# Kernel optimization log

Hardware: AMD Instinct MI355X
Metric: run time of the kernel (lower is better)

Reference implementation:

```python
import jax, jax.numpy as jnp
import numpy as np

T = 3          # num_node_type
B = 8          # batch
N = 512        # max_doc_len
F_IN = 256     # in_features
F_OUT = 128    # out_features
NE = 10        # num_edge_type (embedding has NE+1 rows, row 0 = padding)
ALPHA = 0.2    # leaky relu slope
NEG = -9e15    # masked-score fill, same constant as torch source


def setup_inputs() -> dict:
    key = jax.random.key(0)
    ks = jax.random.split(key, 7)
    node_rep = jax.random.normal(ks[0], (B, N, F_IN), jnp.float32)
    node_type_mask_rep = jax.random.uniform(ks[1], (T, B, N, 1), jnp.float32)
    adj = jax.random.randint(ks[2], (B, N, N), 0, NE + 1, jnp.int32)
    W = jax.random.normal(ks[3], (T, F_IN, F_OUT), jnp.float32) * 0.05
    b = jnp.zeros((T, F_OUT), jnp.float32)
    # attention vector a in R^{2F} split into halves (GAT trick): a([h_i, x2_ij]) = h_i.a1 + x2_ij.a2 + a_b
    a1 = jax.random.normal(ks[4], (F_OUT,), jnp.float32) * 0.05
    a2 = jax.random.normal(ks[5], (F_OUT,), jnp.float32) * 0.05
    a_b = jnp.zeros((), jnp.float32)
    emb = jax.random.normal(ks[6], (NE + 1, F_OUT), jnp.float32) * 0.05
    emb = emb.at[0].set(0.0)  # padding_idx=0
    return {"node_rep": node_rep, "node_type_mask_rep": node_type_mask_rep,
            "adj": adj, "W": W, "b": b, "a1": a1, "a2": a2, "a_b": a_b, "emb": emb}


def reference(node_rep, node_type_mask_rep, adj, W, b, a1, a2, a_b, emb):
    # typed projection: h = sum_t (node_rep @ W_t + b_t) * mask_t   -> (B, N, F_OUT)
    h = jnp.sum((jnp.einsum('bni,tio->tbno', node_rep, W) + b[:, None, None, :])
                * node_type_mask_rep, axis=0)
    # edge-type embeddings: (B, N, N, F_OUT)
    E = emb[adj]
    # x_2[b,i,j] = h[b,j] + E[b,i,j]
    x2 = h[:, None, :, :] + E
    # score[b,i,j] = leakyrelu(a1.h_i + a2.x2_ij + a_b)  (decomposed concat-linear)
    s = (jnp.einsum('bif,f->bi', h, a1)[:, :, None]
         + jnp.einsum('bijf,f->bij', x2, a2) + a_b)
    s = jnp.where(s > 0, s, ALPHA * s)
    s = jnp.where(adj > 0, s, jnp.float32(NEG))
    attn = jax.nn.softmax(s, axis=2)
    # weighted sum over neighbors of x_2 (NOT h), then ELU
    out = jnp.einsum('bij,bijf->bif', attn, x2)
    return jax.nn.elu(out)
```

## Files before the change

### kernel.cpp

```cpp
#include <hip/hip_runtime.h>

constexpr int kB    = 8;
constexpr int kN    = 512;
constexpr int kFIN  = 256;
constexpr int kFOUT = 128;
constexpr int kNE   = 10;
constexpr int kBN   = kB * kN;
constexpr float kALPHA = 0.2f;
constexpr float kNEG   = -9e15f;

__global__ __launch_bounds__(512) void proj_kernel(
    const float* __restrict__ node_rep,
    const float* __restrict__ mask,
    const float* __restrict__ W,
    const float* __restrict__ bias,
    const float* __restrict__ a1,
    const float* __restrict__ a2,
    const float* __restrict__ a_b,
    const float* __restrict__ emb,
    float* __restrict__ h,
    float* __restrict__ s1,
    float* __restrict__ s2,
    float* __restrict__ emb_a2)
{
    __shared__ float xs[8][kFIN];
    __shared__ float parts[9][8][kFOUT];

    const int tid  = threadIdx.x;
    const int row0 = blockIdx.x * 8;
    const int o    = tid & 127;
    const int kq   = tid >> 7;

    {
        const int r = tid >> 6, q = tid & 63;
        *(float4*)&xs[r][q * 4] =
            *(const float4*)&node_rep[(size_t)(row0 + r) * kFIN + q * 4];
    }
    __syncthreads();

    float acc[3][8];
    #pragma unroll
    for (int t = 0; t < 3; ++t)
        #pragma unroll
        for (int r = 0; r < 8; ++r) acc[t][r] = 0.f;

    const float* Wo = W + o;
    #pragma unroll 2
    for (int i4 = 0; i4 < 16; ++i4) {
        const int kb = kq * 64 + i4 * 4;
        float4 xv[8];
        #pragma unroll
        for (int r = 0; r < 8; ++r)
            xv[r] = *(const float4*)&xs[r][kb];
        #pragma unroll
        for (int c = 0; c < 4; ++c) {
            const int k = kb + c;
            const float w0 = Wo[(0 * kFIN + k) * kFOUT];
            const float w1 = Wo[(1 * kFIN + k) * kFOUT];
            const float w2 = Wo[(2 * kFIN + k) * kFOUT];
            #pragma unroll
            for (int r = 0; r < 8; ++r) {
                const float x = ((const float*)&xv[r])[c];
                acc[0][r] = fmaf(w0, x, acc[0][r]);
                acc[1][r] = fmaf(w1, x, acc[1][r]);
                acc[2][r] = fmaf(w2, x, acc[2][r]);
            }
        }
    }

    if (kq > 0) {
        #pragma unroll
        for (int t = 0; t < 3; ++t)
            #pragma unroll
            for (int r = 0; r < 8; ++r)
                parts[(kq - 1) * 3 + t][r][o] = acc[t][r];
    }
    __syncthreads();

    if (kq == 0) {
        #pragma unroll
        for (int r = 0; r < 8; ++r) {
            const int row = row0 + r;
            float hv = 0.f;
            #pragma unroll
            for (int t = 0; t < 3; ++t) {
                const float s = acc[t][r] + parts[t][r][o] + parts[3 + t][r][o]
                              + parts[6 + t][r][o] + bias[t * kFOUT + o];
                hv = fmaf(mask[t * kBN + row], s, hv);
            }
            h[(size_t)row * kFOUT + o] = hv;
            parts[0][r][o] = hv;
        }
    }
    __syncthreads();

    {
        const int r = tid >> 6, lane = tid & 63;
        const float v0 = parts[0][r][lane];
        const float v1 = parts[0][r][64 + lane];
        float p1 = v0 * a1[lane] + v1 * a1[64 + lane];
        float p2 = v0 * a2[lane] + v1 * a2[64 + lane];
        #pragma unroll
        for (int off = 32; off; off >>= 1) {
            p1 += __shfl_down(p1, off);
            p2 += __shfl_down(p2, off);
        }
        if (lane == 0) {
            s1[row0 + r] = p1 + a_b[0];
            s2[row0 + r] = p2;
        }
    }

    if (blockIdx.x == 0 && tid < 176) {
        const int e = tid >> 4, l = tid & 15;
        float p = 0.f;
        #pragma unroll
        for (int k8 = 0; k8 < 8; ++k8)
            p += emb[e * kFOUT + l + k8 * 16] * a2[l + k8 * 16];
        #pragma unroll
        for (int off = 8; off; off >>= 1) p += __shfl_xor(p, off);
        if (l == 0) emb_a2[e] = p;
    }
}

__global__ __launch_bounds__(512) void attn_kernel(
    const int*   __restrict__ adj,
    const float* __restrict__ emb,
    const float* __restrict__ h,
    const float* __restrict__ s1,
    const float* __restrict__ s2,
    const float* __restrict__ emb_a2g,
    float* __restrict__ out)
{
    __shared__ float sc[8][kN + 4];
    __shared__ int   adjs[8][kN];
    __shared__ float s2s[kN];
    __shared__ float s1s[8];
    __shared__ float wsum[8][16];
    __shared__ float ea2[16];

    const int tid = threadIdx.x;
    const int b   = blockIdx.x >> 6;
    const int i0  = (blockIdx.x & 63) * 8;

    if (tid < 16) ea2[tid] = emb_a2g[tid];
    if (tid < 8)  s1s[tid] = s1[b * kN + i0 + tid];
    s2s[tid] = s2[b * kN + tid];
    __syncthreads();

    const int* adjb = adj + ((size_t)(b * kN + i0)) * kN;
    #pragma unroll
    for (int it = 0; it < 2; ++it) {
        const int idx = tid + it * 512;
        const int r = idx >> 7, jq = idx & 127;
        const int4   av  = *(const int4*)&adjb[(size_t)r * kN + jq * 4];
        const float4 s2v = *(const float4*)&s2s[jq * 4];
        const float  sr  = s1s[r];
        float4 sv;
        float s;
        s = sr + s2v.x + ea2[av.x]; s = s > 0.f ? s : kALPHA * s; sv.x = av.x > 0 ? s : kNEG;
        s = sr + s2v.y + ea2[av.y]; s = s > 0.f ? s : kALPHA * s; sv.y = av.y > 0 ? s : kNEG;
        s = sr + s2v.z + ea2[av.z]; s = s > 0.f ? s : kALPHA * s; sv.z = av.z > 0 ? s : kNEG;
        s = sr + s2v.w + ea2[av.w]; s = s > 0.f ? s : kALPHA * s; sv.w = av.w > 0 ? s : kNEG;
        *(float4*)&sc[r][jq * 4]  = sv;
        *(int4*)&adjs[r][jq * 4]  = av;
    }
    __syncthreads();

    {
        const int r = tid >> 6, lane = tid & 63;
        float v[8]; int av[8];
        #pragma unroll
        for (int k = 0; k < 8; ++k) {
            v[k]  = sc[r][lane + k * 64];
            av[k] = adjs[r][lane + k * 64];
        }
        float m = v[0];
        #pragma unroll
        for (int k = 1; k < 8; ++k) m = fmaxf(m, v[k]);
        #pragma unroll
        for (int off = 32; off; off >>= 1) m = fmaxf(m, __shfl_xor(m, off));
        float sum = 0.f;
        #pragma unroll
        for (int k = 0; k < 8; ++k) { v[k] = __expf(v[k] - m); sum += v[k]; }
        #pragma unroll
        for (int off = 32; off; off >>= 1) sum += __shfl_xor(sum, off);
        const float inv = 1.0f / sum;
        #pragma unroll
        for (int k = 0; k < 8; ++k) {
            v[k] *= inv;
            sc[r][lane + k * 64] = v[k];
        }
        #pragma unroll
        for (int e = 1; e <= kNE; ++e) {
            float p = 0.f;
            #pragma unroll
            for (int k = 0; k < 8; ++k) p += (av[k] == e) ? v[k] : 0.f;
            #pragma unroll
            for (int off = 32; off; off >>= 1) p += __shfl_xor(p, off);
            if (lane == 0) wsum[r][e] = p;
        }
    }
    __syncthreads();

    const int f4 = (tid & 31) * 4;
    const int rs = (tid >> 5) & 7;
    const int jh = tid >> 8;
    const float* hb  = h + ((size_t)(b * kN + jh * 256)) * kFOUT + f4;
    const float* scr = &sc[rs][jh * 256];

    float4 acc = {0.f, 0.f, 0.f, 0.f};
    #pragma unroll 4
    for (int j = 0; j < 256; ++j) {
        const float  w  = scr[j];
        const float4 hv = *(const float4*)&hb[(size_t)j * kFOUT];
        acc.x = fmaf(w, hv.x, acc.x); acc.y = fmaf(w, hv.y, acc.y);
        acc.z = fmaf(w, hv.z, acc.z); acc.w = fmaf(w, hv.w, acc.w);
    }
    __syncthreads();

    float* scratch = (float*)adjs;
    if (jh == 1)
        *(float4*)&scratch[(rs * 32 + (tid & 31)) * 4] = acc;
    __syncthreads();
    if (jh == 0) {
        const float4 o2 = *(const float4*)&scratch[(rs * 32 + (tid & 31)) * 4];
        acc.x += o2.x; acc.y += o2.y; acc.z += o2.z; acc.w += o2.w;
        #pragma unroll
        for (int e = 1; e <= kNE; ++e) {
            const float  wv = wsum[rs][e];
            const float4 ev = *(const float4*)&emb[e * kFOUT + f4];
            acc.x = fmaf(wv, ev.x, acc.x); acc.y = fmaf(wv, ev.y, acc.y);
            acc.z = fmaf(wv, ev.z, acc.z); acc.w = fmaf(wv, ev.w, acc.w);
        }
        acc.x = acc.x > 0.f ? acc.x : expm1f(acc.x);
        acc.y = acc.y > 0.f ? acc.y : expm1f(acc.y);
        acc.z = acc.z > 0.f ? acc.z : expm1f(acc.z);
        acc.w = acc.w > 0.f ? acc.w : expm1f(acc.w);
        *(float4*)&out[((size_t)(b * kN + i0 + rs)) * kFOUT + f4] = acc;
    }
}

extern "C" void kernel_launch(void* const* d_in, const int* in_sizes, int n_in,
                              void* d_out, int out_size, void* d_ws, size_t ws_size,
                              hipStream_t stream) {
    const float* node_rep = (const float*)d_in[0];
    const float* mask     = (const float*)d_in[1];
    const int*   adj      = (const int*)  d_in[2];
    const float* W        = (const float*)d_in[3];
    const float* bias     = (const float*)d_in[4];
    const float* a1       = (const float*)d_in[5];
    const float* a2       = (const float*)d_in[6];
    const float* a_b      = (const float*)d_in[7];
    const float* emb      = (const float*)d_in[8];
    float* out = (float*)d_out;

    float* ws     = (float*)d_ws;
    float* h      = ws;
    float* s1     = h + (size_t)kBN * kFOUT;
    float* s2     = s1 + kBN;
    float* emb_a2 = s2 + kBN;

    proj_kernel<<<kBN / 8, 512, 0, stream>>>(
        node_rep, mask, W, bias, a1, a2, a_b, emb, h, s1, s2, emb_a2);
    attn_kernel<<<kBN / 8, 512, 0, stream>>>(
        adj, emb, h, s1, s2, emb_a2, out);
}
```

Measured before the change: 128.5 us.

## Halve block size, register-block attention aggregation over 4 rows, double-buffer W loads

Both kernels move from 512 to 256 threads per block. In the projection, each thread covers twice the K range, and W loads are double-buffered in registers so the next chunk is fetched while the current one is multiplied. In the attention kernel, the softmax weights are stored transposed so each thread reads four rows' weights as one float4 and accumulates four output rows per h load. This cuts global/L2 reads of h by a factor of four per block, at the cost of more registers and an extra shared-memory partial-sum reduction.

```diff
diff --git a/kernel.cpp b/kernel.cpp
--- a/kernel.cpp
+++ b/kernel.cpp
@@ -9,7 +9,7 @@
 constexpr float kALPHA = 0.2f;
 constexpr float kNEG   = -9e15f;
 
-__global__ __launch_bounds__(512) void proj_kernel(
+__global__ __launch_bounds__(256) void proj_kernel(
     const float* __restrict__ node_rep,
     const float* __restrict__ mask,
     const float* __restrict__ W,
@@ -24,15 +24,17 @@
     float* __restrict__ emb_a2)
 {
     __shared__ float xs[8][kFIN];
-    __shared__ float parts[9][8][kFOUT];
+    __shared__ float parts[3][8][kFOUT];
 
     const int tid  = threadIdx.x;
     const int row0 = blockIdx.x * 8;
     const int o    = tid & 127;
     const int kq   = tid >> 7;
 
-    {
-        const int r = tid >> 6, q = tid & 63;
+    #pragma unroll
+    for (int it = 0; it < 2; ++it) {
+        const int idx = tid + it * 256;
+        const int r = idx >> 6, q = idx & 63;
         *(float4*)&xs[r][q * 4] =
             *(const float4*)&node_rep[(size_t)(row0 + r) * kFIN + q * 4];
     }
@@ -45,35 +47,46 @@
         for (int r = 0; r < 8; ++r) acc[t][r] = 0.f;
 
     const float* Wo = W + o;
-    #pragma unroll 2
-    for (int i4 = 0; i4 < 16; ++i4) {
-        const int kb = kq * 64 + i4 * 4;
+    const int k0 = kq * 128;
+
+    float wA[3][4], wB[3][4];
+    auto loadw = [&](float (&buf)[3][4], int kk) {
+        #pragma unroll
+        for (int t = 0; t < 3; ++t)
+            #pragma unroll
+            for (int c = 0; c < 4; ++c)
+                buf[t][c] = Wo[(t * kFIN + kk + c) * kFOUT];
+    };
+    auto fmab = [&](float (&buf)[3][4], int kb) {
         float4 xv[8];
         #pragma unroll
         for (int r = 0; r < 8; ++r)
             xv[r] = *(const float4*)&xs[r][kb];
         #pragma unroll
-        for (int c = 0; c < 4; ++c) {
-            const int k = kb + c;
-            const float w0 = Wo[(0 * kFIN + k) * kFOUT];
-            const float w1 = Wo[(1 * kFIN + k) * kFOUT];
-            const float w2 = Wo[(2 * kFIN + k) * kFOUT];
+        for (int c = 0; c < 4; ++c)
             #pragma unroll
             for (int r = 0; r < 8; ++r) {
                 const float x = ((const float*)&xv[r])[c];
-                acc[0][r] = fmaf(w0, x, acc[0][r]);
-                acc[1][r] = fmaf(w1, x, acc[1][r]);
-                acc[2][r] = fmaf(w2, x, acc[2][r]);
-            }
-        }
-    }
-
-    if (kq > 0) {
+                acc[0][r] = fmaf(buf[0][c], x, acc[0][r]);
+                acc[1][r] = fmaf(buf[1][c], x, acc[1][r]);
+                acc[2][r] = fmaf(buf[2][c], x, acc[2][r]);
+            }
+    };
+
+    loadw(wA, k0);
+    for (int i4 = 0; i4 < 32; i4 += 2) {
+        loadw(wB, k0 + (i4 + 1) * 4);
+        fmab(wA, k0 + i4 * 4);
+        if (i4 + 2 < 32) loadw(wA, k0 + (i4 + 2) * 4);
+        fmab(wB, k0 + (i4 + 1) * 4);
+    }
+
+    if (kq == 1) {
         #pragma unroll
         for (int t = 0; t < 3; ++t)
             #pragma unroll
             for (int r = 0; r < 8; ++r)
-                parts[(kq - 1) * 3 + t][r][o] = acc[t][r];
+                parts[t][r][o] = acc[t][r];
     }
     __syncthreads();
 
@@ -84,8 +97,7 @@
             float hv = 0.f;
             #pragma unroll
             for (int t = 0; t < 3; ++t) {
-                const float s = acc[t][r] + parts[t][r][o] + parts[3 + t][r][o]
-                              + parts[6 + t][r][o] + bias[t * kFOUT + o];
+                const float s = acc[t][r] + parts[t][r][o] + bias[t * kFOUT + o];
                 hv = fmaf(mask[t * kBN + row], s, hv);
             }
             h[(size_t)row * kFOUT + o] = hv;
@@ -95,19 +107,23 @@
     __syncthreads();
 
     {
-        const int r = tid >> 6, lane = tid & 63;
-        const float v0 = parts[0][r][lane];
-        const float v1 = parts[0][r][64 + lane];
-        float p1 = v0 * a1[lane] + v1 * a1[64 + lane];
-        float p2 = v0 * a2[lane] + v1 * a2[64 + lane];
-        #pragma unroll
-        for (int off = 32; off; off >>= 1) {
-            p1 += __shfl_down(p1, off);
-            p2 += __shfl_down(p2, off);
-        }
-        if (lane == 0) {
-            s1[row0 + r] = p1 + a_b[0];
-            s2[row0 + r] = p2;
+        const int wv = tid >> 6, lane = tid & 63;
+        #pragma unroll
+        for (int rr = 0; rr < 2; ++rr) {
+            const int r = wv * 2 + rr;
+            const float v0 = parts[0][r][lane];
+            const float v1 = parts[0][r][64 + lane];
+            float p1 = v0 * a1[lane] + v1 * a1[64 + lane];
+            float p2 = v0 * a2[lane] + v1 * a2[64 + lane];
+            #pragma unroll
+            for (int off = 32; off; off >>= 1) {
+                p1 += __shfl_down(p1, off);
+                p2 += __shfl_down(p2, off);
+            }
+            if (lane == 0) {
+                s1[row0 + r] = p1 + a_b[0];
+                s2[row0 + r] = p2;
+            }
         }
     }
 
@@ -123,7 +139,7 @@
     }
 }
 
-__global__ __launch_bounds__(512) void attn_kernel(
+__global__ __launch_bounds__(256) void attn_kernel(
     const int*   __restrict__ adj,
     const float* __restrict__ emb,
     const float* __restrict__ h,
@@ -134,8 +150,7 @@
 {
     __shared__ float sc[8][kN + 4];
     __shared__ int   adjs[8][kN];
-    __shared__ float s2s[kN];
-    __shared__ float s1s[8];
+    __shared__ float scT[kN][8];
     __shared__ float wsum[8][16];
     __shared__ float ea2[16];
 
@@ -144,100 +159,120 @@
     const int i0  = (blockIdx.x & 63) * 8;
 
     if (tid < 16) ea2[tid] = emb_a2g[tid];
-    if (tid < 8)  s1s[tid] = s1[b * kN + i0 + tid];
-    s2s[tid] = s2[b * kN + tid];
-    __syncthreads();
-
-    const int* adjb = adj + ((size_t)(b * kN + i0)) * kN;
+    __syncthreads();
+
+    const int*   adjb = adj + ((size_t)(b * kN + i0)) * kN;
+    const float* s2b  = s2 + b * kN;
     #pragma unroll
-    for (int it = 0; it < 2; ++it) {
-        const int idx = tid + it * 512;
+    for (int it = 0; it < 4; ++it) {
+        const int idx = tid + it * 256;
         const int r = idx >> 7, jq = idx & 127;
         const int4   av  = *(const int4*)&adjb[(size_t)r * kN + jq * 4];
-        const float4 s2v = *(const float4*)&s2s[jq * 4];
-        const float  sr  = s1s[r];
-        float4 sv;
-        float s;
+        const float4 s2v = *(const float4*)&s2b[jq * 4];
+        const float  sr  = s1[b * kN + i0 + r];
+        float4 sv; float s;
         s = sr + s2v.x + ea2[av.x]; s = s > 0.f ? s : kALPHA * s; sv.x = av.x > 0 ? s : kNEG;
         s = sr + s2v.y + ea2[av.y]; s = s > 0.f ? s : kALPHA * s; sv.y = av.y > 0 ? s : kNEG;
         s = sr + s2v.z + ea2[av.z]; s = s > 0.f ? s : kALPHA * s; sv.z = av.z > 0 ? s : kNEG;
         s = sr + s2v.w + ea2[av.w]; s = s > 0.f ? s : kALPHA * s; sv.w = av.w > 0 ? s : kNEG;
-        *(float4*)&sc[r][jq * 4]  = sv;
-        *(int4*)&adjs[r][jq * 4]  = av;
+        *(float4*)&sc[r][jq * 4] = sv;
+        *(int4*)&adjs[r][jq * 4] = av;
     }
     __syncthreads();
 
     {
-        const int r = tid >> 6, lane = tid & 63;
-        float v[8]; int av[8];
-        #pragma unroll
-        for (int k = 0; k < 8; ++k) {
-            v[k]  = sc[r][lane + k * 64];
-            av[k] = adjs[r][lane + k * 64];
-        }
-        float m = v[0];
-        #pragma unroll
-        for (int k = 1; k < 8; ++k) m = fmaxf(m, v[k]);
-        #pragma unroll
-        for (int off = 32; off; off >>= 1) m = fmaxf(m, __shfl_xor(m, off));
-        float sum = 0.f;
-        #pragma unroll
-        for (int k = 0; k < 8; ++k) { v[k] = __expf(v[k] - m); sum += v[k]; }
-        #pragma unroll
-        for (int off = 32; off; off >>= 1) sum += __shfl_xor(sum, off);
-        const float inv = 1.0f / sum;
-        #pragma unroll
-        for (int k = 0; k < 8; ++k) {
-            v[k] *= inv;
-            sc[r][lane + k * 64] = v[k];
+        const int wv = tid >> 6, lane = tid & 63;
+        #pragma unroll
+        for (int rr = 0; rr < 2; ++rr) {
+            const int r = wv * 2 + rr;
+            float v[8]; int av[8];
+            #pragma unroll
+            for (int k = 0; k < 8; ++k) {
+                v[k]  = sc[r][lane + k * 64];
+                av[k] = adjs[r][lane + k * 64];
+            }
+            float m = v[0];
+            #pragma unroll
+            for (int k = 1; k < 8; ++k) m = fmaxf(m, v[k]);
+            #pragma unroll
+            for (int off = 32; off; off >>= 1) m = fmaxf(m, __shfl_xor(m, off));
+            float sum = 0.f;
+            #pragma unroll
+            for (int k = 0; k < 8; ++k) { v[k] = __expf(v[k] - m); sum += v[k]; }
+            #pragma unroll
+            for (int off = 32; off; off >>= 1) sum += __shfl_xor(sum, off);
+            const float inv = 1.0f / sum;
+            #pragma unroll
+            for (int k = 0; k < 8; ++k) {
+                v[k] *= inv;
+                scT[lane + k * 64][r] = v[k];
+            }
+            #pragma unroll
+            for (int e = 1; e <= kNE; ++e) {
+                float p = 0.f;
+                #pragma unroll
+                for (int k = 0; k < 8; ++k) p += (av[k] == e) ? v[k] : 0.f;
+                #pragma unroll
+                for (int off = 32; off; off >>= 1) p += __shfl_xor(p, off);
+                if (lane == 0) wsum[r][e] = p;
+            }
+        }
+    }
+    __syncthreads();
+
+    const int f4l = tid & 31;
+    const int rg  = (tid >> 5) & 1;
+    const int js  = tid >> 6;
+    const float* hb  = h + ((size_t)(b * kN + js * 128)) * kFOUT + f4l * 4;
+    const float* sct = &scT[js * 128][rg * 4];
+
+    float4 acc0 = {0,0,0,0}, acc1 = {0,0,0,0}, acc2 = {0,0,0,0}, acc3 = {0,0,0,0};
+    #pragma unroll 4
+    for (int jj = 0; jj < 128; ++jj) {
+        const float4 w4 = *(const float4*)&sct[jj * 8];
+        const float4 hv = *(const float4*)&hb[(size_t)jj * kFOUT];
+        acc0.x = fmaf(w4.x, hv.x, acc0.x); acc0.y = fmaf(w4.x, hv.y, acc0.y);
+        acc0.z = fmaf(w4.x, hv.z, acc0.z); acc0.w = fmaf(w4.x, hv.w, acc0.w);
+        acc1.x = fmaf(w4.y, hv.x, acc1.x); acc1.y = fmaf(w4.y, hv.y, acc1.y);
+        acc1.z = fmaf(w4.y, hv.z, acc1.z); acc1.w = fmaf(w4.y, hv.w, acc1.w);
+        acc2.x = fmaf(w4.z, hv.x, acc2.x); acc2.y = fmaf(w4.z, hv.y, acc2.y);
+        acc2.z = fmaf(w4.z, hv.z, acc2.z); acc2.w = fmaf(w4.z, hv.w, acc2.w);
+        acc3.x = fmaf(w4.w, hv.x, acc3.x); acc3.y = fmaf(w4.w, hv.y, acc3.y);
+        acc3.z = fmaf(w4.w, hv.z, acc3.z); acc3.w = fmaf(w4.w, hv.w, acc3.w);
+    }
+    __syncthreads();
+
+    float* parts = (float*)adjs;
+    {
+        const int rbase = rg * 4;
+        *(float4*)&parts[((js * 8) + rbase + 0) * kFOUT + f4l * 4] = acc0;
+        *(float4*)&parts[((js * 8) + rbase + 1) * kFOUT + f4l * 4] = acc1;
+        *(float4*)&parts[((js * 8) + rbase + 2) * kFOUT + f4l * 4] = acc2;
+        *(float4*)&parts[((js * 8) + rbase + 3) * kFOUT + f4l * 4] = acc3;
+    }
+    __syncthreads();
+
+    {
+        const int r  = tid >> 5;
+        const int fl = (tid & 31) * 4;
+        float4 a = {0,0,0,0};
+        #pragma unroll
+        for (int p = 0; p < 4; ++p) {
+            const float4 pv = *(const float4*)&parts[((p * 8) + r) * kFOUT + fl];
+            a.x += pv.x; a.y += pv.y; a.z += pv.z; a.w += pv.w;
         }
         #pragma unroll
         for (int e = 1; e <= kNE; ++e) {
-            float p = 0.f;
-            #pragma unroll
-            for (int k = 0; k < 8; ++k) p += (av[k] == e) ? v[k] : 0.f;
-            #pragma unroll
-            for (int off = 32; off; off >>= 1) p += __shfl_xor(p, off);
-            if (lane == 0) wsum[r][e] = p;
-        }
-    }
-    __syncthreads();
-
-    const int f4 = (tid & 31) * 4;
-    const int rs = (tid >> 5) & 7;
-    const int jh = tid >> 8;
-    const float* hb  = h + ((size_t)(b * kN + jh * 256)) * kFOUT + f4;
-    const float* scr = &sc[rs][jh * 256];
-
-    float4 acc = {0.f, 0.f, 0.f, 0.f};
-    #pragma unroll 4
-    for (int j = 0; j < 256; ++j) {
-        const float  w  = scr[j];
-        const float4 hv = *(const float4*)&hb[(size_t)j * kFOUT];
-        acc.x = fmaf(w, hv.x, acc.x); acc.y = fmaf(w, hv.y, acc.y);
-        acc.z = fmaf(w, hv.z, acc.z); acc.w = fmaf(w, hv.w, acc.w);
-    }
-    __syncthreads();
-
-    float* scratch = (float*)adjs;
-    if (jh == 1)
-        *(float4*)&scratch[(rs * 32 + (tid & 31)) * 4] = acc;
-    __syncthreads();
-    if (jh == 0) {
-        const float4 o2 = *(const float4*)&scratch[(rs * 32 + (tid & 31)) * 4];
-        acc.x += o2.x; acc.y += o2.y; acc.z += o2.z; acc.w += o2.w;
-        #pragma unroll
-        for (int e = 1; e <= kNE; ++e) {
-            const float  wv = wsum[rs][e];
-            const float4 ev = *(const float4*)&emb[e * kFOUT + f4];
-            acc.x = fmaf(wv, ev.x, acc.x); acc.y = fmaf(wv, ev.y, acc.y);
-            acc.z = fmaf(wv, ev.z, acc.z); acc.w = fmaf(wv, ev.w, acc.w);
-        }
-        acc.x = acc.x > 0.f ? acc.x : expm1f(acc.x);
-        acc.y = acc.y > 0.f ? acc.y : expm1f(acc.y);
-        acc.z = acc.z > 0.f ? acc.z : expm1f(acc.z);
-        acc.w = acc.w > 0.f ? acc.w : expm1f(acc.w);
-        *(float4*)&out[((size_t)(b * kN + i0 + rs)) * kFOUT + f4] = acc;
+            const float  wv = wsum[r][e];
+            const float4 ev = *(const float4*)&emb[e * kFOUT + fl];
+            a.x = fmaf(wv, ev.x, a.x); a.y = fmaf(wv, ev.y, a.y);
+            a.z = fmaf(wv, ev.z, a.z); a.w = fmaf(wv, ev.w, a.w);
+        }
+        a.x = a.x > 0.f ? a.x : expm1f(a.x);
+        a.y = a.y > 0.f ? a.y : expm1f(a.y);
+        a.z = a.z > 0.f ? a.z : expm1f(a.z);
+        a.w = a.w > 0.f ? a.w : expm1f(a.w);
+        *(float4*)&out[((size_t)(b * kN + i0 + r)) * kFOUT + fl] = a;
     }
 }
 
@@ -261,8 +296,8 @@
     float* s2     = s1 + kBN;
     float* emb_a2 = s2 + kBN;
 
-    proj_kernel<<<kBN / 8, 512, 0, stream>>>(
+    proj_kernel<<<kBN / 8, 256, 0, stream>>>(
         node_rep, mask, W, bias, a1, a2, a_b, emb, h, s1, s2, emb_a2);
-    attn_kernel<<<kBN / 8, 512, 0, stream>>>(
+    attn_kernel<<<kBN / 8, 256, 0, stream>>>(
         adj, emb, h, s1, s2, emb_a2, out);
 }
```

Result: faster. 112.9 us (-12.1%).
